# Performance work log

Hardware: AMD Instinct MI355X
Metric: run time of the kernel (lower is better)

## Reference

```python
import jax, jax.numpy as jnp
import numpy as np

H = 5  # LSTM hidden size


def _lstm_layer(x, Wih, Whh, bih, bhh):
    # x: [B, T, D]; Wih: [4H, D]; Whh: [4H, H]; biases: [4H]
    B, T, _ = x.shape
    # precompute input contribution with one big GEMM (torch gate order i,f,g,o)
    xg = jnp.einsum('btd,gd->btg', x, Wih) + bih + bhh  # [B,T,4H]
    xg = jnp.swapaxes(xg, 0, 1)  # [T,B,4H]
    WhhT = Whh.T

    def step(carry, g_t):
        h, c = carry
        g = g_t + h @ WhhT
        i, f, gg, o = jnp.split(g, 4, axis=-1)
        i = jax.nn.sigmoid(i)
        f = jax.nn.sigmoid(f)
        gg = jnp.tanh(gg)
        o = jax.nn.sigmoid(o)
        c = f * c + i * gg
        h = o * jnp.tanh(c)
        return (h, c), h

    h0 = jnp.zeros((B, H), x.dtype)
    c0 = jnp.zeros((B, H), x.dtype)
    _, hs = jax.lax.scan(step, (h0, c0), xg)
    return jnp.swapaxes(hs, 0, 1)  # [B,T,H]


def _stacked_lstm(x, params):
    for (Wih, Whh, bih, bhh) in params:
        x = _lstm_layer(x, Wih, Whh, bih, bhh)
    return x


def setup_inputs() -> dict:
    key = jax.random.key(0)
    ks = jax.random.split(key, 24)
    B, T, D = 512, 1024, 225
    s = 1.0 / np.sqrt(H)

    def u(k, shape):
        return jax.random.uniform(k, shape, jnp.float32, -s, s)

    inp = {"x": jax.random.normal(ks[0], (B, T, D), jnp.float32)}
    # lstm1: layer0 input D=225, layer1 input H=5
    inp["l1_Wih0"] = u(ks[1], (4 * H, D)); inp["l1_Whh0"] = u(ks[2], (4 * H, H))
    inp["l1_bih0"] = u(ks[3], (4 * H,)); inp["l1_bhh0"] = u(ks[4], (4 * H,))
    inp["l1_Wih1"] = u(ks[5], (4 * H, H)); inp["l1_Whh1"] = u(ks[6], (4 * H, H))
    inp["l1_bih1"] = u(ks[7], (4 * H,)); inp["l1_bhh1"] = u(ks[8], (4 * H,))
    inp["fc1_W"] = u(ks[9], (H, H)); inp["fc1_b"] = u(ks[10], (H,))
    # lstm2: both layers input H=5
    inp["l2_Wih0"] = u(ks[11], (4 * H, H)); inp["l2_Whh0"] = u(ks[12], (4 * H, H))
    inp["l2_bih0"] = u(ks[13], (4 * H,)); inp["l2_bhh0"] = u(ks[14], (4 * H,))
    inp["l2_Wih1"] = u(ks[15], (4 * H, H)); inp["l2_Whh1"] = u(ks[16], (4 * H, H))
    inp["l2_bih1"] = u(ks[17], (4 * H,)); inp["l2_bhh1"] = u(ks[18], (4 * H,))
    inp["fc2_W"] = u(ks[19], (H, H)); inp["fc2_b"] = u(ks[20], (H,))
    return inp


def reference(x, l1_Wih0, l1_Whh0, l1_bih0, l1_bhh0,
              l1_Wih1, l1_Whh1, l1_bih1, l1_bhh1,
              fc1_W, fc1_b,
              l2_Wih0, l2_Whh0, l2_bih0, l2_bhh0,
              l2_Wih1, l2_Whh1, l2_bih1, l2_bhh1,
              fc2_W, fc2_b):
    # dropout layers are identity in inference mode
    h = _stacked_lstm(x, [(l1_Wih0, l1_Whh0, l1_bih0, l1_bhh0),
                          (l1_Wih1, l1_Whh1, l1_bih1, l1_bhh1)])
    h = jax.nn.relu(h @ fc1_W.T + fc1_b)
    h = _stacked_lstm(h, [(l2_Wih0, l2_Whh0, l2_bih0, l2_bhh0),
                          (l2_Wih1, l2_Whh1, l2_bih1, l2_bhh1)])
    return jax.nn.sigmoid(h @ fc2_W.T + fc2_b)
```

## Files before the change

kernel.cpp:

```cpp
#include <hip/hip_runtime.h>
#include <math.h>

#define T_STEPS 1024
#define B_SIZE  512
#define D_IN    225
#define LOG2E   1.4426950408889634f

typedef float f32x2 __attribute__((ext_vector_type(2)));

__device__ __forceinline__ float fexp2(float x) {
#if __has_builtin(__builtin_amdgcn_exp2f)
  return __builtin_amdgcn_exp2f(x);
#else
  return exp2f(x);
#endif
}
__device__ __forceinline__ float frcp(float x) {
#if __has_builtin(__builtin_amdgcn_rcpf)
  return __builtin_amdgcn_rcpf(x);
#else
  return 1.0f / x;
#endif
}
#define SIG(x) frcp(1.0f + fexp2((x) * (-LOG2E)))
#define TH(x)  fmaf(2.0f, frcp(1.0f + fexp2((x) * (-2.0f * LOG2E))), -1.0f)

#define GL16(gp, lp) __builtin_amdgcn_global_load_lds(                          \
    (const __attribute__((address_space(1))) void*)(gp),                        \
    (__attribute__((address_space(3))) void*)(lp), 16, 0, 0)
#define GL4(gp, lp)  __builtin_amdgcn_global_load_lds(                          \
    (const __attribute__((address_space(1))) void*)(gp),                        \
    (__attribute__((address_space(3))) void*)(lp), 4, 0, 0)

#define WAIT_VM0() do {                                                         \
    asm volatile("s_waitcnt vmcnt(0)" ::: "memory");                            \
    __builtin_amdgcn_sched_barrier(0);                                          \
  } while (0)

__global__ __launch_bounds__(256)
void prep_wt(const float* __restrict__ Wih, const float* __restrict__ bih,
             const float* __restrict__ bhh, float* __restrict__ wt2)
{
  int i = blockIdx.x * 256 + threadIdx.x;
  float v = 0.f;
  if (i < 4500) {
    int k = i / 20, g = i - k * 20;
    v = Wih[g * D_IN + k];
  } else if (i < 4520) {
    v = bih[i - 4500] + bhh[i - 4500];
  }
  wt2[i] = v;
}

__global__ __launch_bounds__(256)
void lstm_fused(const float* __restrict__ x, const float* __restrict__ wtg,
              float* __restrict__ out,
              const float* __restrict__ l1_Whh0,
              const float* __restrict__ l1_Wih1, const float* __restrict__ l1_Whh1,
              const float* __restrict__ l1_bih1, const float* __restrict__ l1_bhh1,
              const float* __restrict__ fc1_W,  const float* __restrict__ fc1_b,
              const float* __restrict__ l2_Wih0, const float* __restrict__ l2_Whh0,
              const float* __restrict__ l2_bih0, const float* __restrict__ l2_bhh0,
              const float* __restrict__ l2_Wih1, const float* __restrict__ l2_Whh1,
              const float* __restrict__ l2_bih1, const float* __restrict__ l2_bhh1,
              const float* __restrict__ fc2_W,  const float* __restrict__ fc2_b)
{
  __shared__ __align__(16) float xq[2][2][1280];
  __shared__ __align__(16) float xsl[2][14400];
  __shared__ __align__(16) float wt[4608];
  __shared__ float outb[2][64][5];
  const int tid   = threadIdx.x;
  const int lane  = tid & 63;
  const int wv    = tid >> 6;
  const int half  = lane >> 5;
  const int l32   = lane & 31;
  const int stage = (l32 < 30) ? (l32 / 5) : 6;
  const int u     = (l32 < 30) ? (l32 - stage * 5) : 0;
  const int b0    = blockIdx.x * 2;

  const bool is_l0   = (stage == 0);
  const bool is_relu = (stage == 2);
  const bool is_fc   = (stage == 2) || (stage == 5);
  const bool is_fc2  = (stage == 5);

  float wi[4][5] = {}, wh[4][5] = {}, bs[4] = {};
  if (stage == 0) {
#pragma unroll
    for (int q = 0; q < 4; ++q)
#pragma unroll
      for (int j = 0; j < 5; ++j) wh[q][j] = l1_Whh0[(u + 5 * q) * 5 + j];
  } else if (stage == 1) {
#pragma unroll
    for (int q = 0; q < 4; ++q) {
#pragma unroll
      for (int j = 0; j < 5; ++j) {
        wi[q][j] = l1_Wih1[(u + 5 * q) * 5 + j];
        wh[q][j] = l1_Whh1[(u + 5 * q) * 5 + j];
      }
      bs[q] = l1_bih1[u + 5 * q] + l1_bhh1[u + 5 * q];
    }
  } else if (stage == 3) {
#pragma unroll
    for (int q = 0; q < 4; ++q) {
#pragma unroll
      for (int j = 0; j < 5; ++j) {
        wi[q][j] = l2_Wih0[(u + 5 * q) * 5 + j];
        wh[q][j] = l2_Whh0[(u + 5 * q) * 5 + j];
      }
      bs[q] = l2_bih0[u + 5 * q] + l2_bhh0[u + 5 * q];
    }
  } else if (stage == 4) {
#pragma unroll
    for (int q = 0; q < 4; ++q) {
#pragma unroll
      for (int j = 0; j < 5; ++j) {
        wi[q][j] = l2_Wih1[(u + 5 * q) * 5 + j];
        wh[q][j] = l2_Whh1[(u + 5 * q) * 5 + j];
      }
      bs[q] = l2_bih1[u + 5 * q] + l2_bhh1[u + 5 * q];
    }
  } else if (stage == 2) {
#pragma unroll
    for (int j = 0; j < 5; ++j) wi[0][j] = fc1_W[u * 5 + j];
    bs[0] = fc1_b[u];
  } else if (stage == 5) {
#pragma unroll
    for (int j = 0; j < 5; ++j) wi[0][j] = fc2_W[u * 5 + j];
    bs[0] = fc2_b[u];
  }

  f32x2 wi01[5], wi23[5], wh01[5], wh23[5];
#pragma unroll
  for (int j = 0; j < 5; ++j) {
    wi01[j] = f32x2{wi[0][j], wi[1][j]};
    wi23[j] = f32x2{wi[2][j], wi[3][j]};
    wh01[j] = f32x2{wh[0][j], wh[1][j]};
    wh23[j] = f32x2{wh[2][j], wh[3][j]};
  }
  const f32x2 bs01 = f32x2{bs[0], bs[1]};
  const f32x2 bs23 = f32x2{bs[2], bs[3]};

  int ii[5], ih[5];
  const int bse = half * 32;
  const int inb = (stage >= 1 && stage <= 5) ? (stage - 1) * 5 : 0;
  const int hb_ = (stage <= 5) ? stage * 5 : 0;
#pragma unroll
  for (int j = 0; j < 5; ++j) {
    ii[j] = (bse + inb + j) * 4;
    ih[j] = (bse + hb_ + j) * 4;
  }

  const float* obf = &outb[0][0][0];
  float* outbase = out + (size_t)b0 * T_STEPS * 5;
  int lof[10], ofs[10];
  bool fg1[10], fg2[10];
#pragma unroll
  for (int i2 = 0; i2 < 10; ++i2) {
    int idx = i2 * 64 + lane;
    int e  = (idx >= 320) ? 1 : 0;
    int r  = idx - e * 320;
    int tq = r / 5;
    int j2 = r - tq * 5;
    lof[i2] = e * 320 + (((tq - 5) & 63) * 5) + j2;
    ofs[i2] = e * (T_STEPS * 5) + tq * 5 + j2;
    fg1[i2] = (tq >= 5);
    fg2[i2] = (tq < 5);
  }

#define AG(G) (((G) & 1) ? acc2[(G) >> 1].y : acc2[(G) >> 1].x)
#define PRODUCE(CH, BUF)                                                       \
  { const int e_ = wv - 1;                                                     \
    const float* slab_ = x + ((size_t)(b0 + e_) * T_STEPS + (CH) * 64) * 225;  \
    float* dst_ = &xsl[e_][0];                                                 \
    _Pragma("unroll")                                                          \
    for (int m_ = 0; m_ < 56; ++m_)                                            \
      GL16(slab_ + m_ * 256 + lane * 4, dst_ + m_ * 256);                      \
    GL4(slab_ + 14336 + lane, dst_ + 14336);                                   \
    WAIT_VM0();                                                                \
    f32x2 acc2[10];                                                            \
    _Pragma("unroll")                                                          \
    for (int p_ = 0; p_ < 10; ++p_)                                            \
      acc2[p_] = f32x2{wt[4500 + 2 * p_], wt[4500 + 2 * p_ + 1]};              \
    const float* xr_ = dst_ + lane * 225;                                      \
    _Pragma("unroll 3")                                                        \
    for (int k_ = 0; k_ < 225; ++k_) {                                         \
      const float xv_ = xr_[k_];                                               \
      const f32x2 xv2_ = f32x2{xv_, xv_};                                      \
      const float* wk_ = wt + k_ * 20;                                         \
      const float4 wA_ = *(const float4*)(wk_);                                \
      const float4 wB_ = *(const float4*)(wk_ + 4);                            \
      const float4 wC_ = *(const float4*)(wk_ + 8);                            \
      const float4 wD_ = *(const float4*)(wk_ + 12);                           \
      const float4 wE_ = *(const float4*)(wk_ + 16);                           \
      acc2[0] = __builtin_elementwise_fma(f32x2{wA_.x, wA_.y}, xv2_, acc2[0]); \
      acc2[1] = __builtin_elementwise_fma(f32x2{wA_.z, wA_.w}, xv2_, acc2[1]); \
      acc2[2] = __builtin_elementwise_fma(f32x2{wB_.x, wB_.y}, xv2_, acc2[2]); \
      acc2[3] = __builtin_elementwise_fma(f32x2{wB_.z, wB_.w}, xv2_, acc2[3]); \
      acc2[4] = __builtin_elementwise_fma(f32x2{wC_.x, wC_.y}, xv2_, acc2[4]); \
      acc2[5] = __builtin_elementwise_fma(f32x2{wC_.z, wC_.w}, xv2_, acc2[5]); \
      acc2[6] = __builtin_elementwise_fma(f32x2{wD_.x, wD_.y}, xv2_, acc2[6]); \
      acc2[7] = __builtin_elementwise_fma(f32x2{wD_.z, wD_.w}, xv2_, acc2[7]); \
      acc2[8] = __builtin_elementwise_fma(f32x2{wE_.x, wE_.y}, xv2_, acc2[8]); \
      acc2[9] = __builtin_elementwise_fma(f32x2{wE_.z, wE_.w}, xv2_, acc2[9]); \
    }                                                                          \
    float* qp_ = &xq[BUF][e_][lane * 20];                                      \
    _Pragma("unroll")                                                          \
    for (int u_ = 0; u_ < 5; ++u_) {                                           \
      float4 o_;                                                               \
      o_.x = AG(u_);      o_.y = AG(5 + u_);                                   \
      o_.z = AG(10 + u_); o_.w = AG(15 + u_);                                  \
      *(float4*)(qp_ + 4 * u_) = o_;                                           \
    } }

#define TICK(QV, GUARDED, KVAL)                                                \
  { const int hvi_ = __float_as_int(hv);                                       \
    float inx[5], hhx[5];                                                      \
    _Pragma("unroll")                                                          \
    for (int j = 0; j < 5; ++j) {                                              \
      inx[j] = __int_as_float(__builtin_amdgcn_ds_bpermute(ii[j], hvi_));      \
      hhx[j] = __int_as_float(__builtin_amdgcn_ds_bpermute(ih[j], hvi_));      \
    }                                                                          \
    f32x2 a01 = is_l0 ? f32x2{(QV).x, (QV).y} : bs01;                          \
    f32x2 a23 = is_l0 ? f32x2{(QV).z, (QV).w} : bs23;                          \
    f32x2 b01, b23;                                                            \
    { const f32x2 h0 = f32x2{hhx[0], hhx[0]};                                  \
      b01 = wh01[0] * h0; b23 = wh23[0] * h0; }                                \
    _Pragma("unroll")                                                          \
    for (int j = 0; j < 5; ++j) {                                              \
      const f32x2 xj = f32x2{inx[j], inx[j]};                                  \
      a01 = __builtin_elementwise_fma(wi01[j], xj, a01);                       \
      a23 = __builtin_elementwise_fma(wi23[j], xj, a23);                       \
    }                                                                          \
    _Pragma("unroll")                                                          \
    for (int j = 1; j < 5; ++j) {                                              \
      const f32x2 hj = f32x2{hhx[j], hhx[j]};                                  \
      b01 = __builtin_elementwise_fma(wh01[j], hj, b01);                       \
      b23 = __builtin_elementwise_fma(wh23[j], hj, b23);                       \
    }                                                                          \
    const f32x2 pre01 = a01 + b01, pre23 = a23 + b23;                          \
    float i_ = SIG(pre01.x), f_ = SIG(pre01.y);                                \
    float g_ = TH(pre23.x),  o_ = SIG(pre23.y);                                \
    float cn = fmaf(f_, c, i_ * g_);                                           \
    float hl = o_ * TH(cn);                                                    \
    float fx = is_relu ? fmaxf(pre01.x, 0.0f) : i_;                            \
    float hn = is_fc ? fx : hl;                                                \
    if (GUARDED) { bool ok = (KVAL) >= stage; c = ok ? cn : c; hv = ok ? hn : hv; } \
    else         { c = cn; hv = hn; }                                          \
    if (is_fc2) outb[half][((KVAL) + 59) & 63][u] = i_;                        \
  }

#define LQ(T) (*(const float4*)(xqb + 20 * (T)))
#define MINQ(X) (((X) > 63) ? 63 : (X))

#define CHUNK_BODY(GUARDED)                                                    \
  { float4 qA = LQ(0), qB = LQ(1), qC = LQ(2), qD = LQ(3);                     \
    _Pragma("unroll")                                                          \
    for (int g4 = 0; g4 < 16; ++g4) {                                          \
      const int kk = g4 * 4;                                                   \
      TICK(qA, GUARDED, kk + 0)                                                \
      qA = LQ(MINQ(kk + 4));                                                   \
      TICK(qB, GUARDED, kk + 1)                                                \
      qB = LQ(MINQ(kk + 5));                                                   \
      TICK(qC, GUARDED, kk + 2)                                                \
      qC = LQ(MINQ(kk + 6));                                                   \
      TICK(qD, GUARDED, kk + 3)                                                \
      qD = LQ(MINQ(kk + 7));                                                   \
    } }

#define FLUSH(TBASE, MODE)                                                     \
  { _Pragma("unroll")                                                          \
    for (int i2 = 0; i2 < 10; ++i2) {                                          \
      float v = obf[lof[i2]];                                                  \
      bool ok = (MODE == 0) || ((MODE == 1) ? fg1[i2] : fg2[i2]);              \
      if (ok) outbase[ofs[i2] + (TBASE) * 5] = v;                              \
    } }

  float hv = 0.f, c = 0.f;

  if (wv == 1 || wv == 2) {
    for (int m = wv - 1; m < 18; m += 2)
      GL16(wtg + m * 256 + lane * 4, wt + m * 256);
    WAIT_VM0();
  }
  __syncthreads();
  if (wv == 1 || wv == 2) PRODUCE(0, 0)
  __syncthreads();

  for (int ch = 0; ch < 16; ++ch) {
    if (wv == 0) {
      const float* xqb = &xq[ch & 1][half][4 * u];
      if (ch == 0) {
        CHUNK_BODY(true)
        FLUSH(-5, 1)
      } else {
        CHUNK_BODY(false)
        FLUSH(ch * 64 - 5, 0)
      }
    } else if ((wv == 1 || wv == 2) && ch < 15) {
      PRODUCE(ch + 1, (ch + 1) & 1)
    }
    __syncthreads();
  }
  if (wv == 0) {
    const float* xqb = &xq[0][half][4 * u];
    float4 qZ = LQ(0);
    TICK(qZ, false, 0)
    TICK(qZ, false, 1)
    TICK(qZ, false, 2)
    TICK(qZ, false, 3)
    TICK(qZ, false, 4)
    FLUSH(T_STEPS - 5, 2)
  }

#undef AG
#undef PRODUCE
#undef TICK
#undef LQ
#undef MINQ
#undef CHUNK_BODY
#undef FLUSH
}

extern "C" void kernel_launch(void* const* d_in, const int* in_sizes, int n_in,
                              void* d_out, int out_size, void* d_ws, size_t ws_size,
                              hipStream_t stream)
{
  const float* x        = (const float*)d_in[0];
  const float* l1_Wih0  = (const float*)d_in[1];
  const float* l1_Whh0  = (const float*)d_in[2];
  const float* l1_bih0  = (const float*)d_in[3];
  const float* l1_bhh0  = (const float*)d_in[4];
  const float* l1_Wih1  = (const float*)d_in[5];
  const float* l1_Whh1  = (const float*)d_in[6];
  const float* l1_bih1  = (const float*)d_in[7];
  const float* l1_bhh1  = (const float*)d_in[8];
  const float* fc1_W    = (const float*)d_in[9];
  const float* fc1_b    = (const float*)d_in[10];
  const float* l2_Wih0  = (const float*)d_in[11];
  const float* l2_Whh0  = (const float*)d_in[12];
  const float* l2_bih0  = (const float*)d_in[13];
  const float* l2_bhh0  = (const float*)d_in[14];
  const float* l2_Wih1  = (const float*)d_in[15];
  const float* l2_Whh1  = (const float*)d_in[16];
  const float* l2_bih1  = (const float*)d_in[17];
  const float* l2_bhh1  = (const float*)d_in[18];
  const float* fc2_W    = (const float*)d_in[19];
  const float* fc2_b    = (const float*)d_in[20];

  float* wtws = (float*)d_ws;
  float* out  = (float*)d_out;

  prep_wt<<<dim3(18), dim3(256), 0, stream>>>(l1_Wih0, l1_bih0, l1_bhh0, wtws);

  lstm_fused<<<dim3(B_SIZE / 2), dim3(256), 0, stream>>>(
      x, wtws, out, l1_Whh0, l1_Wih1, l1_Whh1, l1_bih1, l1_bhh1,
      fc1_W, fc1_b, l2_Wih0, l2_Whh0, l2_bih0, l2_bhh0,
      l2_Wih1, l2_Whh1, l2_bih1, l2_bhh1, fc2_W, fc2_b);
}
```

Before: 350.5 us.

## Alternate producer waves per chunk, each computing both batch rows' input projections

```diff
diff --git a/kernel.cpp b/kernel.cpp
--- a/kernel.cpp
+++ b/kernel.cpp
@@ -52,7 +52,7 @@
   wt2[i] = v;
 }
 
-__global__ __launch_bounds__(256)
+__global__ __launch_bounds__(192)
 void lstm_fused(const float* __restrict__ x, const float* __restrict__ wtg,
               float* __restrict__ out,
               const float* __restrict__ l1_Whh0,
@@ -167,49 +167,71 @@
     fg2[i2] = (tq < 5);
   }
 
-#define AG(G) (((G) & 1) ? acc2[(G) >> 1].y : acc2[(G) >> 1].x)
+#define AGA(G) (((G) & 1) ? acA[(G) >> 1].y : acA[(G) >> 1].x)
+#define AGB(G) (((G) & 1) ? acB[(G) >> 1].y : acB[(G) >> 1].x)
 #define PRODUCE(CH, BUF)                                                       \
-  { const int e_ = wv - 1;                                                     \
-    const float* slab_ = x + ((size_t)(b0 + e_) * T_STEPS + (CH) * 64) * 225;  \
-    float* dst_ = &xsl[e_][0];                                                 \
+  { const float* s0_ = x + ((size_t)(b0 + 0) * T_STEPS + (CH) * 64) * 225;     \
+    const float* s1_ = x + ((size_t)(b0 + 1) * T_STEPS + (CH) * 64) * 225;     \
     _Pragma("unroll")                                                          \
     for (int m_ = 0; m_ < 56; ++m_)                                            \
-      GL16(slab_ + m_ * 256 + lane * 4, dst_ + m_ * 256);                      \
-    GL4(slab_ + 14336 + lane, dst_ + 14336);                                   \
+      GL16(s0_ + m_ * 256 + lane * 4, &xsl[0][m_ * 256]);                      \
+    GL4(s0_ + 14336 + lane, &xsl[0][14336]);                                   \
+    _Pragma("unroll")                                                          \
+    for (int m_ = 0; m_ < 56; ++m_)                                            \
+      GL16(s1_ + m_ * 256 + lane * 4, &xsl[1][m_ * 256]);                      \
+    GL4(s1_ + 14336 + lane, &xsl[1][14336]);                                   \
     WAIT_VM0();                                                                \
-    f32x2 acc2[10];                                                            \
-    _Pragma("unroll")                                                          \
-    for (int p_ = 0; p_ < 10; ++p_)                                            \
-      acc2[p_] = f32x2{wt[4500 + 2 * p_], wt[4500 + 2 * p_ + 1]};              \
-    const float* xr_ = dst_ + lane * 225;                                      \
+    f32x2 acA[10], acB[10];                                                    \
+    _Pragma("unroll")                                                          \
+    for (int p_ = 0; p_ < 10; ++p_) {                                          \
+      acA[p_] = f32x2{wt[4500 + 2 * p_], wt[4500 + 2 * p_ + 1]};               \
+      acB[p_] = acA[p_];                                                       \
+    }                                                                          \
     _Pragma("unroll 3")                                                        \
     for (int k_ = 0; k_ < 225; ++k_) {                                         \
-      const float xv_ = xr_[k_];                                               \
-      const f32x2 xv2_ = f32x2{xv_, xv_};                                      \
-      const float* wk_ = wt + k_ * 20;                                         \
-      const float4 wA_ = *(const float4*)(wk_);                                \
-      const float4 wB_ = *(const float4*)(wk_ + 4);                            \
-      const float4 wC_ = *(const float4*)(wk_ + 8);                            \
-      const float4 wD_ = *(const float4*)(wk_ + 12);                           \
-      const float4 wE_ = *(const float4*)(wk_ + 16);                           \
-      acc2[0] = __builtin_elementwise_fma(f32x2{wA_.x, wA_.y}, xv2_, acc2[0]); \
-      acc2[1] = __builtin_elementwise_fma(f32x2{wA_.z, wA_.w}, xv2_, acc2[1]); \
-      acc2[2] = __builtin_elementwise_fma(f32x2{wB_.x, wB_.y}, xv2_, acc2[2]); \
-      acc2[3] = __builtin_elementwise_fma(f32x2{wB_.z, wB_.w}, xv2_, acc2[3]); \
-      acc2[4] = __builtin_elementwise_fma(f32x2{wC_.x, wC_.y}, xv2_, acc2[4]); \
-      acc2[5] = __builtin_elementwise_fma(f32x2{wC_.z, wC_.w}, xv2_, acc2[5]); \
-      acc2[6] = __builtin_elementwise_fma(f32x2{wD_.x, wD_.y}, xv2_, acc2[6]); \
-      acc2[7] = __builtin_elementwise_fma(f32x2{wD_.z, wD_.w}, xv2_, acc2[7]); \
-      acc2[8] = __builtin_elementwise_fma(f32x2{wE_.x, wE_.y}, xv2_, acc2[8]); \
-      acc2[9] = __builtin_elementwise_fma(f32x2{wE_.z, wE_.w}, xv2_, acc2[9]); \
-    }                                                                          \
-    float* qp_ = &xq[BUF][e_][lane * 20];                                      \
+      const float xa_ = xsl[0][lane * 225 + k_];                               \
+      const float xb_ = xsl[1][lane * 225 + k_];                               \
+      const f32x2 va_ = f32x2{xa_, xa_}, vb_ = f32x2{xb_, xb_};                \
+      const float4 wA_ = *(const float4*)(&wt[k_ * 20]);                       \
+      const float4 wB_ = *(const float4*)(&wt[k_ * 20 + 4]);                   \
+      const float4 wC_ = *(const float4*)(&wt[k_ * 20 + 8]);                   \
+      const float4 wD_ = *(const float4*)(&wt[k_ * 20 + 12]);                  \
+      const float4 wE_ = *(const float4*)(&wt[k_ * 20 + 16]);                  \
+      const f32x2 w0_ = f32x2{wA_.x, wA_.y}, w1_ = f32x2{wA_.z, wA_.w};        \
+      const f32x2 w2_ = f32x2{wB_.x, wB_.y}, w3_ = f32x2{wB_.z, wB_.w};        \
+      const f32x2 w4_ = f32x2{wC_.x, wC_.y}, w5_ = f32x2{wC_.z, wC_.w};        \
+      const f32x2 w6_ = f32x2{wD_.x, wD_.y}, w7_ = f32x2{wD_.z, wD_.w};        \
+      const f32x2 w8_ = f32x2{wE_.x, wE_.y}, w9_ = f32x2{wE_.z, wE_.w};        \
+      acA[0] = __builtin_elementwise_fma(w0_, va_, acA[0]);                    \
+      acB[0] = __builtin_elementwise_fma(w0_, vb_, acB[0]);                    \
+      acA[1] = __builtin_elementwise_fma(w1_, va_, acA[1]);                    \
+      acB[1] = __builtin_elementwise_fma(w1_, vb_, acB[1]);                    \
+      acA[2] = __builtin_elementwise_fma(w2_, va_, acA[2]);                    \
+      acB[2] = __builtin_elementwise_fma(w2_, vb_, acB[2]);                    \
+      acA[3] = __builtin_elementwise_fma(w3_, va_, acA[3]);                    \
+      acB[3] = __builtin_elementwise_fma(w3_, vb_, acB[3]);                    \
+      acA[4] = __builtin_elementwise_fma(w4_, va_, acA[4]);                    \
+      acB[4] = __builtin_elementwise_fma(w4_, vb_, acB[4]);                    \
+      acA[5] = __builtin_elementwise_fma(w5_, va_, acA[5]);                    \
+      acB[5] = __builtin_elementwise_fma(w5_, vb_, acB[5]);                    \
+      acA[6] = __builtin_elementwise_fma(w6_, va_, acA[6]);                    \
+      acB[6] = __builtin_elementwise_fma(w6_, vb_, acB[6]);                    \
+      acA[7] = __builtin_elementwise_fma(w7_, va_, acA[7]);                    \
+      acB[7] = __builtin_elementwise_fma(w7_, vb_, acB[7]);                    \
+      acA[8] = __builtin_elementwise_fma(w8_, va_, acA[8]);                    \
+      acB[8] = __builtin_elementwise_fma(w8_, vb_, acB[8]);                    \
+      acA[9] = __builtin_elementwise_fma(w9_, va_, acA[9]);                    \
+      acB[9] = __builtin_elementwise_fma(w9_, vb_, acB[9]);                    \
+    }                                                                          \
     _Pragma("unroll")                                                          \
     for (int u_ = 0; u_ < 5; ++u_) {                                           \
-      float4 o_;                                                               \
-      o_.x = AG(u_);      o_.y = AG(5 + u_);                                   \
-      o_.z = AG(10 + u_); o_.w = AG(15 + u_);                                  \
-      *(float4*)(qp_ + 4 * u_) = o_;                                           \
+      float4 oa_, ob_;                                                         \
+      oa_.x = AGA(u_);      oa_.y = AGA(5 + u_);                               \
+      oa_.z = AGA(10 + u_); oa_.w = AGA(15 + u_);                              \
+      ob_.x = AGB(u_);      ob_.y = AGB(5 + u_);                               \
+      ob_.z = AGB(10 + u_); ob_.w = AGB(15 + u_);                              \
+      *(float4*)(&xq[BUF][0][lane * 20 + 4 * u_]) = oa_;                       \
+      *(float4*)(&xq[BUF][1][lane * 20 + 4 * u_]) = ob_;                       \
     } }
 
 #define TICK(QV, GUARDED, KVAL)                                                \
@@ -277,18 +299,21 @@
 
   float hv = 0.f, c = 0.f;
 
+  if (wv == 0) __builtin_amdgcn_s_setprio(1);
+
   if (wv == 1 || wv == 2) {
     for (int m = wv - 1; m < 18; m += 2)
-      GL16(wtg + m * 256 + lane * 4, wt + m * 256);
+      GL16(wtg + m * 256 + lane * 4, &wt[m * 256]);
     WAIT_VM0();
   }
   __syncthreads();
-  if (wv == 1 || wv == 2) PRODUCE(0, 0)
+  if (wv == 1) PRODUCE(0, 0)
   __syncthreads();
 
-  for (int ch = 0; ch < 16; ++ch) {
+  for (int ch2 = 0; ch2 < 8; ++ch2) {
+    const int ch = ch2 * 2;
     if (wv == 0) {
-      const float* xqb = &xq[ch & 1][half][4 * u];
+      const float* xqb = &xq[0][half][4 * u];
       if (ch == 0) {
         CHUNK_BODY(true)
         FLUSH(-5, 1)
@@ -296,8 +321,16 @@
         CHUNK_BODY(false)
         FLUSH(ch * 64 - 5, 0)
       }
-    } else if ((wv == 1 || wv == 2) && ch < 15) {
-      PRODUCE(ch + 1, (ch + 1) & 1)
+    } else if (wv == 1) {
+      PRODUCE(ch + 1, 1)
+    }
+    __syncthreads();
+    if (wv == 0) {
+      const float* xqb = &xq[1][half][4 * u];
+      CHUNK_BODY(false)
+      FLUSH((ch + 1) * 64 - 5, 0)
+    } else if (wv == 2) {
+      if (ch < 14) PRODUCE(ch + 2, 0)
     }
     __syncthreads();
   }
@@ -312,7 +345,8 @@
     FLUSH(T_STEPS - 5, 2)
   }
 
-#undef AG
+#undef AGA
+#undef AGB
 #undef PRODUCE
 #undef TICK
 #undef LQ
@@ -352,7 +386,7 @@
 
   prep_wt<<<dim3(18), dim3(256), 0, stream>>>(l1_Wih0, l1_bih0, l1_bhh0, wtws);
 
-  lstm_fused<<<dim3(B_SIZE / 2), dim3(256), 0, stream>>>(
+  lstm_fused<<<dim3(B_SIZE / 2), dim3(192), 0, stream>>>(
       x, wtws, out, l1_Whh0, l1_Wih1, l1_Whh1, l1_bih1, l1_bhh1,
       fc1_W, fc1_b, l2_Wih0, l2_Whh0, l2_bih0, l2_bhh0,
       l2_Wih1, l2_Whh1, l2_bih1, l2_bhh1, fc2_W, fc2_b);
```

Measured after the change: 420.9 us. 20.1% more time.
